# Kernel optimization log

Hardware: AMD Instinct MI355X
Metric: run time of the kernel (lower is better)

The kernel has to match this reference:

```python
import jax, jax.numpy as jnp
import numpy as np

B, S, W = 32, 512, 8
CHAR_EMB = 100
SUB_EMB = 100
LSTM_H = 400          # total bidirectional hidden; 200 per direction
HD = LSTM_H // 2
CHAR_V = 10000
BICHAR_V = 400000
PRE_V = 500000        # pretrained subword vocab
SUB_V = 100000        # trainable subword table (init_num)
N_LABELS = 4
UNK = 1


def setup_inputs() -> dict:
    key = jax.random.key(0)
    ks = jax.random.split(key, 16)
    sc = 0.05
    inp = {
        # values in [1, vocab) so there are no pad(=0) tokens -> full-length sequences
        "chars": jax.random.randint(ks[0], (B, S), 1, CHAR_V),
        "bichars": jax.random.randint(ks[1], (B, S), 1, BICHAR_V),
        "subwords": jax.random.randint(ks[2], (B, S - 2, W), 1, PRE_V),
        "emb_char_w": jax.random.normal(ks[3], (CHAR_V, CHAR_EMB), jnp.float32) * sc,
        "emb_bichar_w": jax.random.normal(ks[4], (BICHAR_V, CHAR_EMB), jnp.float32) * sc,
        "emb_subword_w": jax.random.normal(ks[5], (SUB_V, SUB_EMB), jnp.float32) * sc,
        "pretrained_w": jax.random.normal(ks[6], (PRE_V, SUB_EMB), jnp.float32) * sc,
        # PyTorch LSTM params (gate order i,f,g,o); b = b_ih + b_hh folded
        "Wih_f": jax.random.normal(ks[7], (4 * HD, 2 * CHAR_EMB), jnp.float32) * sc,
        "Whh_f": jax.random.normal(ks[8], (4 * HD, HD), jnp.float32) * sc,
        "b_f": jax.random.normal(ks[9], (4 * HD,), jnp.float32) * sc,
        "Wih_b": jax.random.normal(ks[10], (4 * HD, 2 * CHAR_EMB), jnp.float32) * sc,
        "Whh_b": jax.random.normal(ks[11], (4 * HD, HD), jnp.float32) * sc,
        "b_b": jax.random.normal(ks[12], (4 * HD,), jnp.float32) * sc,
        "ffn_w": jax.random.normal(ks[13], (N_LABELS, LSTM_H + SUB_EMB), jnp.float32) * sc,
        "ffn_b": jax.random.normal(ks[14], (N_LABELS,), jnp.float32) * sc,
    }
    return inp


def _lstm_dir(x, Wih, Whh, b):
    # x: [B,S,I] -> [B,S,HD], single direction, zero init state
    xg = jnp.einsum('bsi,gi->bsg', x, Wih) + b  # [B,S,4HD]
    h0 = jnp.zeros((x.shape[0], Whh.shape[1]), x.dtype)

    def step(carry, xt):
        h, c = carry
        g = xt + h @ Whh.T
        i, f, gg, o = jnp.split(g, 4, axis=-1)
        c = jax.nn.sigmoid(f) * c + jax.nn.sigmoid(i) * jnp.tanh(gg)
        h = jax.nn.sigmoid(o) * jnp.tanh(c)
        return (h, c), h

    _, hs = jax.lax.scan(step, (h0, h0), jnp.swapaxes(xg, 0, 1))
    return jnp.swapaxes(hs, 0, 1)


def _forward(chars, bichars, subwords, emb_char_w, emb_bichar_w, emb_subword_w,
             pretrained_w, Wih_f, Whh_f, b_f, Wih_b, Whh_b, b_b, ffn_w, ffn_b):
    Sq = chars.shape[1]
    Wl = subwords.shape[2]
    x = jnp.concatenate([emb_char_w[chars], emb_bichar_w[bichars]], axis=-1)  # [B,S,2E]
    hf = _lstm_dir(x, Wih_f, Whh_f, b_f)
    hb = _lstm_dir(x[:, ::-1], Wih_b, Whh_b, b_b)[:, ::-1]
    # span features: equivalent to torch's O(S^2) unsqueeze-subtract + diagonal
    # gather, but computed directly for the W needed diagonals.
    # span[b,k,i] = [ fwd[k+i+1]-fwd[k] , bwd[k+1]-bwd[k+i+2] ], zero if k+i > S-3
    ks_ = jnp.arange(Sq - 2)[:, None]          # span start (in [0, S-3])
    offs = jnp.arange(Wl)[None, :]             # span length - 1
    end = ks_ + offs
    valid = (end <= Sq - 3)
    e1 = jnp.clip(end + 1, 0, Sq - 1)
    e2 = jnp.clip(end + 2, 0, Sq - 1)
    span_f = hf[:, e1] - hf[:, ks_]            # [B,S-2,W,HD]
    span_b = hb[:, ks_ + 1] - hb[:, e2]        # [B,S-2,W,HD]
    span = jnp.concatenate([span_f, span_b], axis=-1) * valid[None, :, :, None]
    # subword embedding: pretrained (full vocab) + trainable (OOV -> unk)
    sub = pretrained_w[subwords] + emb_subword_w[jnp.where(subwords >= SUB_V, UNK, subwords)]
    feat = jnp.concatenate([span, sub], axis=-1)  # [B,S-2,W,LSTM_H+SUB_EMB]
    return feat @ ffn_w.T + ffn_b                 # [B,S-2,W,N_LABELS]


def reference(chars, bichars, subwords, emb_char_w, emb_bichar_w, emb_subword_w,
              pretrained_w, Wih_f, Whh_f, b_f, Wih_b, Whh_b, b_b, ffn_w, ffn_b):
    return _forward(chars, bichars, subwords, emb_char_w, emb_bichar_w, emb_subword_w,
                    pretrained_w, Wih_f, Whh_f, b_f, Wih_b, Whh_b, b_b, ffn_w, ffn_b)
```

## Files before the change

kernel.cpp:

```cpp
#include <hip/hip_runtime.h>
#include <hip/hip_bf16.h>
#include <math.h>

#define B 32
#define S 512
#define W 8
#define CE 100
#define SE 100
#define HD 200
#define G4 800
#define IN2 200
#define SUBV 100000
#define UNK 1
#define NL 4
#define SK (S - 2)
#define FEAT 500

typedef _Float16 h2_t __attribute__((ext_vector_type(2)));

__device__ __forceinline__ float fsig(float x) {
    return 1.f / (1.f + __expf(-x));
}
__device__ __forceinline__ float ftanh(float x) {
    float e = __expf(-2.f * fabsf(x));
    float r = (1.f - e) / (1.f + e);
    return copysignf(r, x);
}

__device__ __forceinline__ float wave_sum64(float v) {
#if __has_builtin(__builtin_amdgcn_update_dpp)
#define DPPADD(C) { int x_ = __builtin_amdgcn_update_dpp(0, __float_as_int(v), C, 0xf, 0xf, true); \
                    v += __int_as_float(x_); }
    DPPADD(0x111)
    DPPADD(0x112)
    DPPADD(0x114)
    DPPADD(0x118)
    DPPADD(0x142)
    DPPADD(0x143)
#undef DPPADD
    return v;
#else
    v += __shfl_xor(v, 1);  v += __shfl_xor(v, 2);  v += __shfl_xor(v, 4);
    v += __shfl_xor(v, 8);  v += __shfl_xor(v, 16); v += __shfl_xor(v, 32);
    return v;
#endif
}

__device__ __forceinline__ float dot4(float4 w, float4 h) {
    return fmaf(w.w, h.w, fmaf(w.z, h.z, fmaf(w.y, h.y, w.x * h.x)));
}

__device__ __forceinline__ float dot2f(unsigned a, unsigned b, float c) {
#if __has_builtin(__builtin_amdgcn_fdot2)
    return __builtin_amdgcn_fdot2(__builtin_bit_cast(h2_t, a),
                                  __builtin_bit_cast(h2_t, b), c, false);
#else
    h2_t x = __builtin_bit_cast(h2_t, a);
    h2_t y = __builtin_bit_cast(h2_t, b);
    return c + (float)x[0] * (float)y[0] + (float)x[1] * (float)y[1];
#endif
}

__global__ void transpose_pack_k(const float* __restrict__ in, unsigned* __restrict__ out) {
    int o = blockIdx.x * 256 + threadIdx.x;
    if (o >= 100 * G4) return;
    int k2 = o / G4, g = o % G4;
    h2_t v;
    v[0] = (_Float16)in[g * 200 + 2 * k2];
    v[1] = (_Float16)in[g * 200 + 2 * k2 + 1];
    out[o] = __builtin_bit_cast(unsigned, v);
}

__global__ void xg_k(const int* __restrict__ chars, const int* __restrict__ bichars,
                     const float* __restrict__ cw, const float* __restrict__ bw,
                     const unsigned* __restrict__ WTh_f, const float* __restrict__ bf,
                     const unsigned* __restrict__ WTh_b, const float* __restrict__ bb,
                     float* __restrict__ xgf, float* __restrict__ xgb) {
    const int dir = blockIdx.y;
    const unsigned* WT = dir ? WTh_b : WTh_f;
    const float* bias  = dir ? bb : bf;
    float* out         = dir ? xgb : xgf;
    int r0 = blockIdx.x * 16;
    __shared__ unsigned xs2[16][100];
    for (int i = threadIdx.x; i < 16 * 100; i += 256) {
        int r = i / 100, c2 = i % 100;
        int row = r0 + r;
        float a, b;
        if (c2 < 50) {
            const float* p = cw + (size_t)chars[row] * CE + 2 * c2;
            a = p[0]; b = p[1];
        } else {
            const float* p = bw + (size_t)bichars[row] * CE + 2 * (c2 - 50);
            a = p[0]; b = p[1];
        }
        h2_t v; v[0] = (_Float16)a; v[1] = (_Float16)b;
        xs2[r][c2] = __builtin_bit_cast(unsigned, v);
    }
    __syncthreads();
    float acc[4][16];
    for (int q = 0; q < 4; q++)
        for (int r = 0; r < 16; r++) acc[q][r] = 0.f;
    int tid = threadIdx.x;
    for (int k2 = 0; k2 < 100; k2++) {
        const unsigned* wrow = WT + (size_t)k2 * G4;
        unsigned w0 = wrow[tid];
        unsigned w1 = wrow[tid + 256];
        unsigned w2 = wrow[tid + 512];
        unsigned w3 = (tid < 32) ? wrow[tid + 768] : 0u;
        for (int r = 0; r < 16; r++) {
            unsigned xv = xs2[r][k2];
            acc[0][r] = dot2f(w0, xv, acc[0][r]);
            acc[1][r] = dot2f(w1, xv, acc[1][r]);
            acc[2][r] = dot2f(w2, xv, acc[2][r]);
            acc[3][r] = dot2f(w3, xv, acc[3][r]);
        }
    }
    for (int q = 0; q < 4; q++) {
        int g = tid + q * 256;
        if (g < G4) {
            float bv = bias[g];
            for (int r = 0; r < 16; r++)
                out[(size_t)(r0 + r) * G4 + g] = acc[q][r] + bv;
        }
    }
}

__global__ __launch_bounds__(1024)
void lstm_k(const float* __restrict__ xgf, const float* __restrict__ xgb,
            const float* __restrict__ Whh_f, const float* __restrict__ Whh_b,
            float* __restrict__ hf, float* __restrict__ hb) {
    __shared__ float4 wlds[5064];
    __shared__ __align__(16) float hsA[256];
    __shared__ __align__(16) float hsB[256];
    __shared__ __align__(16) float gbA[112];
    __shared__ __align__(16) float gbB[112];

    const int blk = blockIdx.x;
    const int sl  = blk >> 5;
    const int pg  = blk & 31;
    const int dir = pg >> 4;
    const int bA  = pg & 15;
    const int bB  = bA + 16;
    const float* xg  = dir ? xgb : xgf;
    const float* Whh = dir ? Whh_b : Whh_f;
    float* hout      = dir ? hb : hf;

    const int t = threadIdx.x;
    const int lane = t & 63;
    const int wid = t >> 6;

    for (int i = t; i < 5064; i += 1024) {
        float4 v = {0.f, 0.f, 0.f, 0.f};
        if (i < 5000) {
            int col = i / 50, l = i - col * 50;
            int row = (col / 25) * 200 + sl * 25 + (col % 25);
            v = *(const float4*)(Whh + (size_t)row * HD + 4 * l);
        }
        wlds[i] = v;
    }
    if (t < 256) { hsA[t] = 0.f; hsB[t] = 0.f; }

    const bool is_act = (t >= 960) && (t < 985);
    const int u = t - 960;
    const bool fill = (t < 200) && (t / 25 != sl);
    float cstA = 0.f, cstB = 0.f;
    float xA0=0,xA1=0,xA2=0,xA3=0, xB0=0,xB1=0,xB2=0,xB3=0;
    if (is_act) {
        int ts0 = dir ? (S - 1) : 0;
        const float* pa = xg + ((size_t)bA * S + ts0) * G4 + sl * 25 + u;
        const float* pb = xg + ((size_t)bB * S + ts0) * G4 + sl * 25 + u;
        xA0 = pa[0]; xA1 = pa[200]; xA2 = pa[400]; xA3 = pa[600];
        xB0 = pb[0]; xB1 = pb[200]; xB2 = pb[400]; xB3 = pb[600];
    }
    __syncthreads();

#define COMPUTE(hsX, gbX)                                                      \
    {                                                                          \
        float4 hv = ((const float4*)hsX)[lane];                                \
        _Pragma("unroll")                                                      \
        for (int j = 0; j < 7; j++) {                                          \
            int c = wid + 15 * j;                                              \
            if (c < 100) {                                                     \
                float4 wv = wlds[c * 50 + lane];                               \
                float a = wave_sum64(dot4(wv, hv));                            \
                if (lane == 63) gbX[c] = a;                                    \
            }                                                                  \
        }                                                                      \
    }

#define POLL(dst, srcp)                                                        \
    {                                                                          \
        float v_;                                                              \
        do { v_ = __hip_atomic_load(srcp, __ATOMIC_RELAXED,                    \
                                    __HIP_MEMORY_SCOPE_AGENT); } while (v_ != v_); \
        dst = v_;                                                              \
    }

    for (int s = 0; s < S; s++) {
        const int ts  = dir ? (S - 1 - s) : s;
        const int tsp = dir ? (S - s)     : (s - 1);
        const int tsn = (s + 1 < S) ? (dir ? (S - 2 - s) : (s + 1)) : ts;

        if (is_act && s > 0) {
            float ig = fsig(gbB[u] + xB0);
            float fg = fsig(gbB[25 + u] + xB1);
            float gt = ftanh(gbB[50 + u] + xB2);
            float og = fsig(gbB[75 + u] + xB3);
            cstB = fg * cstB + ig * gt;
            float h = og * ftanh(cstB);
            hsB[sl * 25 + u] = h;
            __hip_atomic_store(&hout[((size_t)bB * S + tsp) * HD + sl * 25 + u], h,
                               __ATOMIC_RELAXED, __HIP_MEMORY_SCOPE_AGENT);
            const float* pn = xg + ((size_t)bB * S + ts) * G4 + sl * 25 + u;
            xB0 = pn[0]; xB1 = pn[200]; xB2 = pn[400]; xB3 = pn[600];
        }
        if (wid < 15) COMPUTE(hsA, gbA)
        if (s > 0 && fill) POLL(hsB[t], hout + ((size_t)bB * S + tsp) * HD + t)
        __syncthreads();

        if (is_act) {
            float ig = fsig(gbA[u] + xA0);
            float fg = fsig(gbA[25 + u] + xA1);
            float gt = ftanh(gbA[50 + u] + xA2);
            float og = fsig(gbA[75 + u] + xA3);
            cstA = fg * cstA + ig * gt;
            float h = og * ftanh(cstA);
            hsA[sl * 25 + u] = h;
            __hip_atomic_store(&hout[((size_t)bA * S + ts) * HD + sl * 25 + u], h,
                               __ATOMIC_RELAXED, __HIP_MEMORY_SCOPE_AGENT);
            const float* pn = xg + ((size_t)bA * S + tsn) * G4 + sl * 25 + u;
            xA0 = pn[0]; xA1 = pn[200]; xA2 = pn[400]; xA3 = pn[600];
        }
        if (wid < 15) COMPUTE(hsB, gbB)
        if (fill) POLL(hsA[t], hout + ((size_t)bA * S + ts) * HD + t)
        __syncthreads();
    }
    if (is_act) {
        const int tl = dir ? 0 : (S - 1);
        float ig = fsig(gbB[u] + xB0);
        float fg = fsig(gbB[25 + u] + xB1);
        float gt = ftanh(gbB[50 + u] + xB2);
        float og = fsig(gbB[75 + u] + xB3);
        cstB = fg * cstB + ig * gt;
        float h = og * ftanh(cstB);
        __hip_atomic_store(&hout[((size_t)bB * S + tl) * HD + sl * 25 + u], h,
                           __ATOMIC_RELAXED, __HIP_MEMORY_SCOPE_AGENT);
    }
#undef COMPUTE
#undef POLL
}

__global__ void out_k(const int* __restrict__ subwords,
                      const float* __restrict__ pre_w, const float* __restrict__ sub_w,
                      const float* __restrict__ hf, const float* __restrict__ hb,
                      const float* __restrict__ ffn_w, const float* __restrict__ ffn_b,
                      float* __restrict__ out) {
    int wave = (blockIdx.x * 256 + threadIdx.x) >> 6;
    int lane = threadIdx.x & 63;
    if (wave >= B * SK * W) return;
    int i = wave % W;
    int bk = wave / W;
    int k = bk % SK;
    int b = bk / SK;
    int end = k + i;
    float vscale = (end <= S - 3) ? 1.f : 0.f;
    int e1 = min(end + 1, S - 1);
    int e2 = min(end + 2, S - 1);
    const float* hfb = hf + (size_t)b * S * HD;
    const float* hbb = hb + (size_t)b * S * HD;
    int sw = subwords[wave];
    int sw2 = (sw >= SUBV) ? UNK : sw;
    float acc0 = 0, acc1 = 0, acc2 = 0, acc3 = 0;
    for (int j = lane; j < FEAT; j += 64) {
        float fv;
        if (j < HD) {
            fv = (hfb[(size_t)e1 * HD + j] - hfb[(size_t)k * HD + j]) * vscale;
        } else if (j < 2 * HD) {
            int jj = j - HD;
            fv = (hbb[(size_t)(k + 1) * HD + jj] - hbb[(size_t)e2 * HD + jj]) * vscale;
        } else {
            int jj = j - 2 * HD;
            fv = pre_w[(size_t)sw * SE + jj] + sub_w[(size_t)sw2 * SE + jj];
        }
        acc0 += ffn_w[j] * fv;
        acc1 += ffn_w[FEAT + j] * fv;
        acc2 += ffn_w[2 * FEAT + j] * fv;
        acc3 += ffn_w[3 * FEAT + j] * fv;
    }
    for (int off = 32; off; off >>= 1) {
        acc0 += __shfl_down(acc0, off);
        acc1 += __shfl_down(acc1, off);
        acc2 += __shfl_down(acc2, off);
        acc3 += __shfl_down(acc3, off);
    }
    if (lane == 0) {
        float* o = out + (size_t)wave * NL;
        o[0] = acc0 + ffn_b[0];
        o[1] = acc1 + ffn_b[1];
        o[2] = acc2 + ffn_b[2];
        o[3] = acc3 + ffn_b[3];
    }
}

extern "C" void kernel_launch(void* const* d_in, const int* in_sizes, int n_in,
                              void* d_out, int out_size, void* d_ws, size_t ws_size,
                              hipStream_t stream) {
    const int*   chars    = (const int*)d_in[0];
    const int*   bichars  = (const int*)d_in[1];
    const int*   subwords = (const int*)d_in[2];
    const float* cw    = (const float*)d_in[3];
    const float* bw    = (const float*)d_in[4];
    const float* subw  = (const float*)d_in[5];
    const float* prew  = (const float*)d_in[6];
    const float* Wih_f = (const float*)d_in[7];
    const float* Whh_f = (const float*)d_in[8];
    const float* b_f   = (const float*)d_in[9];
    const float* Wih_b = (const float*)d_in[10];
    const float* Whh_b = (const float*)d_in[11];
    const float* b_b   = (const float*)d_in[12];
    const float* ffn_w = (const float*)d_in[13];
    const float* ffn_b = (const float*)d_in[14];
    float* out = (float*)d_out;

    float* ws = (float*)d_ws;
    unsigned* WTh_f = (unsigned*)ws;
    unsigned* WTh_b = WTh_f + 80000;
    float* xgf = (float*)(WTh_b + 80000);
    float* xgb = xgf + 13107200;
    float* hf  = xgb + 13107200;
    float* hb  = hf + 3276800;

    (void)hipMemsetAsync(hf, 0xFF, 2 * 3276800 * sizeof(float), stream);
    transpose_pack_k<<<313, 256, 0, stream>>>(Wih_f, WTh_f);
    transpose_pack_k<<<313, 256, 0, stream>>>(Wih_b, WTh_b);
    xg_k<<<dim3(B * S / 16, 2), 256, 0, stream>>>(chars, bichars, cw, bw,
                                                  WTh_f, b_f, WTh_b, b_b, xgf, xgb);
    lstm_k<<<256, 1024, 0, stream>>>(xgf, xgb, Whh_f, Whh_b, hf, hb);
    out_k<<<(B * SK * W) / 4, 256, 0, stream>>>(subwords, prew, subw, hf, hb, ffn_w, ffn_b, out);
}
```

Baseline: 1.193 ms.

## Split LSTM hidden units across 16 blocks per batch group instead of 8

Moves the persistent recurrent LSTM kernel from 8 slices of 25 hidden units per (direction, batch pair) to 16 slices of 12 or 13 units, launching 512 blocks of 512 threads. Each block handles about half the gate columns per step, so the per-step recurrent dot-product work on the critical path gets shorter. In exchange, each block must poll more remote hidden values from global memory every step, and cross-block synchronisation traffic grows. It also assumes all 512 blocks are co-resident, since blocks spin-wait on each other.

After: 1.265 ms. 1.06x slower.

```diff
diff --git a/kernel.cpp b/kernel.cpp
--- a/kernel.cpp
+++ b/kernel.cpp
@@ -125,15 +125,15 @@
     }
 }
 
-__global__ __launch_bounds__(1024)
+__global__ __launch_bounds__(512)
 void lstm_k(const float* __restrict__ xgf, const float* __restrict__ xgb,
             const float* __restrict__ Whh_f, const float* __restrict__ Whh_b,
             float* __restrict__ hf, float* __restrict__ hb) {
-    __shared__ float4 wlds[5064];
+    __shared__ float4 wlds[4500];
     __shared__ __align__(16) float hsA[256];
     __shared__ __align__(16) float hsB[256];
-    __shared__ __align__(16) float gbA[112];
-    __shared__ __align__(16) float gbB[112];
+    __shared__ __align__(16) float gbA[64];
+    __shared__ __align__(16) float gbB[64];
 
     const int blk = blockIdx.x;
     const int sl  = blk >> 5;
@@ -141,6 +141,9 @@
     const int dir = pg >> 4;
     const int bA  = pg & 15;
     const int bB  = bA + 16;
+    const int U    = (sl < 8) ? 13 : 12;
+    const int base = (sl < 8) ? 13 * sl : 104 + 12 * (sl - 8);
+    const int C    = 4 * U;
     const float* xg  = dir ? xgb : xgf;
     const float* Whh = dir ? Whh_b : Whh_f;
     float* hout      = dir ? hb : hf;
@@ -149,26 +152,27 @@
     const int lane = t & 63;
     const int wid = t >> 6;
 
-    for (int i = t; i < 5064; i += 1024) {
+    for (int i = t; i < 2664; i += 512) {
         float4 v = {0.f, 0.f, 0.f, 0.f};
-        if (i < 5000) {
+        if (i < 50 * C) {
             int col = i / 50, l = i - col * 50;
-            int row = (col / 25) * 200 + sl * 25 + (col % 25);
+            int row = (col / U) * 200 + base + (col % U);
             v = *(const float4*)(Whh + (size_t)row * HD + 4 * l);
         }
         wlds[i] = v;
     }
     if (t < 256) { hsA[t] = 0.f; hsB[t] = 0.f; }
-
-    const bool is_act = (t >= 960) && (t < 985);
-    const int u = t - 960;
-    const bool fill = (t < 200) && (t / 25 != sl);
+    if (t < 64)  { gbA[t] = 0.f; gbB[t] = 0.f; }
+
+    const bool is_act = (t >= 448) && (t < 448 + U);
+    const int u = t - 448;
+    const bool fill = (t < 200) && (t < base || t >= base + U);
     float cstA = 0.f, cstB = 0.f;
     float xA0=0,xA1=0,xA2=0,xA3=0, xB0=0,xB1=0,xB2=0,xB3=0;
     if (is_act) {
         int ts0 = dir ? (S - 1) : 0;
-        const float* pa = xg + ((size_t)bA * S + ts0) * G4 + sl * 25 + u;
-        const float* pb = xg + ((size_t)bB * S + ts0) * G4 + sl * 25 + u;
+        const float* pa = xg + ((size_t)bA * S + ts0) * G4 + base + u;
+        const float* pb = xg + ((size_t)bB * S + ts0) * G4 + base + u;
         xA0 = pa[0]; xA1 = pa[200]; xA2 = pa[400]; xA3 = pa[600];
         xB0 = pb[0]; xB1 = pb[200]; xB2 = pb[400]; xB3 = pb[600];
     }
@@ -178,9 +182,9 @@
     {                                                                          \
         float4 hv = ((const float4*)hsX)[lane];                                \
         _Pragma("unroll")                                                      \
-        for (int j = 0; j < 7; j++) {                                          \
-            int c = wid + 15 * j;                                              \
-            if (c < 100) {                                                     \
+        for (int j = 0; j < 8; j++) {                                          \
+            int c = wid + 7 * j;                                               \
+            if (c < C) {                                                       \
                 float4 wv = wlds[c * 50 + lane];                               \
                 float a = wave_sum64(dot4(wv, hv));                            \
                 if (lane == 63) gbX[c] = a;                                    \
@@ -203,47 +207,47 @@
 
         if (is_act && s > 0) {
             float ig = fsig(gbB[u] + xB0);
-            float fg = fsig(gbB[25 + u] + xB1);
-            float gt = ftanh(gbB[50 + u] + xB2);
-            float og = fsig(gbB[75 + u] + xB3);
+            float fg = fsig(gbB[U + u] + xB1);
+            float gt = ftanh(gbB[2 * U + u] + xB2);
+            float og = fsig(gbB[3 * U + u] + xB3);
             cstB = fg * cstB + ig * gt;
             float h = og * ftanh(cstB);
-            hsB[sl * 25 + u] = h;
-            __hip_atomic_store(&hout[((size_t)bB * S + tsp) * HD + sl * 25 + u], h,
+            hsB[base + u] = h;
+            __hip_atomic_store(&hout[((size_t)bB * S + tsp) * HD + base + u], h,
                                __ATOMIC_RELAXED, __HIP_MEMORY_SCOPE_AGENT);
-            const float* pn = xg + ((size_t)bB * S + ts) * G4 + sl * 25 + u;
+            const float* pn = xg + ((size_t)bB * S + ts) * G4 + base + u;
             xB0 = pn[0]; xB1 = pn[200]; xB2 = pn[400]; xB3 = pn[600];
         }
-        if (wid < 15) COMPUTE(hsA, gbA)
+        if (wid < 7) COMPUTE(hsA, gbA)
         if (s > 0 && fill) POLL(hsB[t], hout + ((size_t)bB * S + tsp) * HD + t)
         __syncthreads();
 
         if (is_act) {
             float ig = fsig(gbA[u] + xA0);
-            float fg = fsig(gbA[25 + u] + xA1);
-            float gt = ftanh(gbA[50 + u] + xA2);
-            float og = fsig(gbA[75 + u] + xA3);
+            float fg = fsig(gbA[U + u] + xA1);
+            float gt = ftanh(gbA[2 * U + u] + xA2);
+            float og = fsig(gbA[3 * U + u] + xA3);
             cstA = fg * cstA + ig * gt;
             float h = og * ftanh(cstA);
-            hsA[sl * 25 + u] = h;
-            __hip_atomic_store(&hout[((size_t)bA * S + ts) * HD + sl * 25 + u], h,
+            hsA[base + u] = h;
+            __hip_atomic_store(&hout[((size_t)bA * S + ts) * HD + base + u], h,
                                __ATOMIC_RELAXED, __HIP_MEMORY_SCOPE_AGENT);
-            const float* pn = xg + ((size_t)bA * S + tsn) * G4 + sl * 25 + u;
+            const float* pn = xg + ((size_t)bA * S + tsn) * G4 + base + u;
             xA0 = pn[0]; xA1 = pn[200]; xA2 = pn[400]; xA3 = pn[600];
         }
-        if (wid < 15) COMPUTE(hsB, gbB)
+        if (wid < 7) COMPUTE(hsB, gbB)
         if (fill) POLL(hsA[t], hout + ((size_t)bA * S + ts) * HD + t)
         __syncthreads();
     }
     if (is_act) {
         const int tl = dir ? 0 : (S - 1);
         float ig = fsig(gbB[u] + xB0);
-        float fg = fsig(gbB[25 + u] + xB1);
-        float gt = ftanh(gbB[50 + u] + xB2);
-        float og = fsig(gbB[75 + u] + xB3);
+        float fg = fsig(gbB[U + u] + xB1);
+        float gt = ftanh(gbB[2 * U + u] + xB2);
+        float og = fsig(gbB[3 * U + u] + xB3);
         cstB = fg * cstB + ig * gt;
         float h = og * ftanh(cstB);
-        __hip_atomic_store(&hout[((size_t)bB * S + tl) * HD + sl * 25 + u], h,
+        __hip_atomic_store(&hout[((size_t)bB * S + tl) * HD + base + u], h,
                            __ATOMIC_RELAXED, __HIP_MEMORY_SCOPE_AGENT);
     }
 #undef COMPUTE
@@ -335,6 +339,6 @@
     transpose_pack_k<<<313, 256, 0, stream>>>(Wih_b, WTh_b);
     xg_k<<<dim3(B * S / 16, 2), 256, 0, stream>>>(chars, bichars, cw, bw,
                                                   WTh_f, b_f, WTh_b, b_b, xgf, xgb);
-    lstm_k<<<256, 1024, 0, stream>>>(xgf, xgb, Whh_f, Whh_b, hf, hb);
+    lstm_k<<<512, 512, 0, stream>>>(xgf, xgb, Whh_f, Whh_b, hf, hb);
     out_k<<<(B * SK * W) / 4, 256, 0, stream>>>(subwords, prew, subw, hf, hb, ffn_w, ffn_b, out);
 }
```

## Lockstep both batch sequences in LSTM recurrence, computing both matvecs per phase

Applied to the files above, without the earlier changes.

The recurrent kernel previously staggered two batch sequences (A and B) across half-steps, so one sequence's matvec overlapped the other's activation and poll. Now both sequences' activations and polls run together in one phase. Both matvecs then run in a second phase across all 16 waves, with each weight load from LDS reused for both dot products. This cuts per-iteration weight LDS traffic and puts the 16th wave to work. The cost is lost overlap: the cross-block poll latency for both sequences now sits on the critical path of the same phase instead of being hidden behind the other sequence's matvec.

Result: slower. 1.580 ms (+32.4%).

```diff
diff --git a/kernel.cpp b/kernel.cpp
--- a/kernel.cpp
+++ b/kernel.cpp
@@ -160,33 +160,21 @@
     }
     if (t < 256) { hsA[t] = 0.f; hsB[t] = 0.f; }
 
-    const bool is_act = (t >= 960) && (t < 985);
-    const int u = t - 960;
-    const bool fill = (t < 200) && (t / 25 != sl);
-    float cstA = 0.f, cstB = 0.f;
-    float xA0=0,xA1=0,xA2=0,xA3=0, xB0=0,xB1=0,xB2=0,xB3=0;
-    if (is_act) {
+    const bool actA = (t >= 960) && (t < 985);
+    const bool actB = (t >= 896) && (t < 921);
+    const int u = actA ? (t - 960) : (t - 896);
+    const bool fillA = (t < 200) && (t / 25 != sl);
+    const int tB = t - 256;
+    const bool fillB = (t >= 256) && (tB < 200) && (tB / 25 != sl);
+    float cst = 0.f;
+    float x0 = 0, x1 = 0, x2 = 0, x3 = 0;
+    if (actA || actB) {
         int ts0 = dir ? (S - 1) : 0;
-        const float* pa = xg + ((size_t)bA * S + ts0) * G4 + sl * 25 + u;
-        const float* pb = xg + ((size_t)bB * S + ts0) * G4 + sl * 25 + u;
-        xA0 = pa[0]; xA1 = pa[200]; xA2 = pa[400]; xA3 = pa[600];
-        xB0 = pb[0]; xB1 = pb[200]; xB2 = pb[400]; xB3 = pb[600];
+        int bX = actA ? bA : bB;
+        const float* p = xg + ((size_t)bX * S + ts0) * G4 + sl * 25 + u;
+        x0 = p[0]; x1 = p[200]; x2 = p[400]; x3 = p[600];
     }
     __syncthreads();
-
-#define COMPUTE(hsX, gbX)                                                      \
-    {                                                                          \
-        float4 hv = ((const float4*)hsX)[lane];                                \
-        _Pragma("unroll")                                                      \
-        for (int j = 0; j < 7; j++) {                                          \
-            int c = wid + 15 * j;                                              \
-            if (c < 100) {                                                     \
-                float4 wv = wlds[c * 50 + lane];                               \
-                float a = wave_sum64(dot4(wv, hv));                            \
-                if (lane == 63) gbX[c] = a;                                    \
-            }                                                                  \
-        }                                                                      \
-    }
 
 #define POLL(dst, srcp)                                                        \
     {                                                                          \
@@ -199,54 +187,58 @@
     for (int s = 0; s < S; s++) {
         const int ts  = dir ? (S - 1 - s) : s;
         const int tsp = dir ? (S - s)     : (s - 1);
-        const int tsn = (s + 1 < S) ? (dir ? (S - 2 - s) : (s + 1)) : ts;
-
-        if (is_act && s > 0) {
-            float ig = fsig(gbB[u] + xB0);
-            float fg = fsig(gbB[25 + u] + xB1);
-            float gt = ftanh(gbB[50 + u] + xB2);
-            float og = fsig(gbB[75 + u] + xB3);
-            cstB = fg * cstB + ig * gt;
-            float h = og * ftanh(cstB);
-            hsB[sl * 25 + u] = h;
-            __hip_atomic_store(&hout[((size_t)bB * S + tsp) * HD + sl * 25 + u], h,
-                               __ATOMIC_RELAXED, __HIP_MEMORY_SCOPE_AGENT);
-            const float* pn = xg + ((size_t)bB * S + ts) * G4 + sl * 25 + u;
-            xB0 = pn[0]; xB1 = pn[200]; xB2 = pn[400]; xB3 = pn[600];
-        }
-        if (wid < 15) COMPUTE(hsA, gbA)
-        if (s > 0 && fill) POLL(hsB[t], hout + ((size_t)bB * S + tsp) * HD + t)
+
+        if (s > 0) {
+            if (actA || actB) {
+                const float* gb = actA ? gbA : gbB;
+                float* hsX = actA ? hsA : hsB;
+                const int bX = actA ? bA : bB;
+                float ig = fsig(gb[u] + x0);
+                float fg = fsig(gb[25 + u] + x1);
+                float gt = ftanh(gb[50 + u] + x2);
+                float og = fsig(gb[75 + u] + x3);
+                cst = fg * cst + ig * gt;
+                float h = og * ftanh(cst);
+                hsX[sl * 25 + u] = h;
+                __hip_atomic_store(&hout[((size_t)bX * S + tsp) * HD + sl * 25 + u],
+                                   h, __ATOMIC_RELAXED, __HIP_MEMORY_SCOPE_AGENT);
+                const float* pn = xg + ((size_t)bX * S + ts) * G4 + sl * 25 + u;
+                x0 = pn[0]; x1 = pn[200]; x2 = pn[400]; x3 = pn[600];
+            }
+            if (fillA) POLL(hsA[t],  hout + ((size_t)bA * S + tsp) * HD + t)
+            if (fillB) POLL(hsB[tB], hout + ((size_t)bB * S + tsp) * HD + tB)
+        }
         __syncthreads();
 
-        if (is_act) {
-            float ig = fsig(gbA[u] + xA0);
-            float fg = fsig(gbA[25 + u] + xA1);
-            float gt = ftanh(gbA[50 + u] + xA2);
-            float og = fsig(gbA[75 + u] + xA3);
-            cstA = fg * cstA + ig * gt;
-            float h = og * ftanh(cstA);
-            hsA[sl * 25 + u] = h;
-            __hip_atomic_store(&hout[((size_t)bA * S + ts) * HD + sl * 25 + u], h,
-                               __ATOMIC_RELAXED, __HIP_MEMORY_SCOPE_AGENT);
-            const float* pn = xg + ((size_t)bA * S + tsn) * G4 + sl * 25 + u;
-            xA0 = pn[0]; xA1 = pn[200]; xA2 = pn[400]; xA3 = pn[600];
-        }
-        if (wid < 15) COMPUTE(hsB, gbB)
-        if (fill) POLL(hsA[t], hout + ((size_t)bA * S + ts) * HD + t)
+        {
+            float4 hvA = ((const float4*)hsA)[lane];
+            float4 hvB = ((const float4*)hsB)[lane];
+            #pragma unroll
+            for (int j = 0; j < 7; j++) {
+                int c = wid + 16 * j;
+                if (c < 100) {
+                    float4 wv = wlds[c * 50 + lane];
+                    float a = wave_sum64(dot4(wv, hvA));
+                    float b = wave_sum64(dot4(wv, hvB));
+                    if (lane == 63) { gbA[c] = a; gbB[c] = b; }
+                }
+            }
+        }
         __syncthreads();
     }
-    if (is_act) {
+    if (actA || actB) {
+        const float* gb = actA ? gbA : gbB;
+        const int bX = actA ? bA : bB;
         const int tl = dir ? 0 : (S - 1);
-        float ig = fsig(gbB[u] + xB0);
-        float fg = fsig(gbB[25 + u] + xB1);
-        float gt = ftanh(gbB[50 + u] + xB2);
-        float og = fsig(gbB[75 + u] + xB3);
-        cstB = fg * cstB + ig * gt;
-        float h = og * ftanh(cstB);
-        __hip_atomic_store(&hout[((size_t)bB * S + tl) * HD + sl * 25 + u], h,
+        float ig = fsig(gb[u] + x0);
+        float fg = fsig(gb[25 + u] + x1);
+        float gt = ftanh(gb[50 + u] + x2);
+        float og = fsig(gb[75 + u] + x3);
+        cst = fg * cst + ig * gt;
+        float h = og * ftanh(cst);
+        __hip_atomic_store(&hout[((size_t)bX * S + tl) * HD + sl * 25 + u], h,
                            __ATOMIC_RELAXED, __HIP_MEMORY_SCOPE_AGENT);
     }
-#undef COMPUTE
 #undef POLL
 }
 
```
